# Performance work log

Hardware: AMD Instinct MI355X
Metric: run time of the kernel (lower is better)

Reference implementation:

```python
import jax, jax.numpy as jnp
import numpy as np
from jax.scipy.special import betainc

B, N, F_IN, D = 128, 50, 64, 64
E = N * (N - 1)          # fully-connected directed graph (no self loops)
S = N - 1                # number of ablation submodels
BN_ = B * N
EPS = 1e-5
NEG = jnp.float32(-1e9)
ALPHA = 0.05
SLOPE = 0.2              # LeakyReLU negative slope in GAT attention


def _build_graph():
    # edges grouped by target p: (c, p) for all c != p
    dst = np.repeat(np.arange(N), N - 1)
    src = np.concatenate([np.concatenate([np.arange(p), np.arange(p + 1, N)]) for p in range(N)])
    return src.astype(np.int64), dst.astype(np.int64)


def setup_inputs():
    key = jax.random.key(0)
    k = jax.random.split(key, 16)
    src, dst = _build_graph()
    edge_index = jnp.asarray(np.stack([src, dst]))
    offs = np.repeat(np.arange(B) * N, E)
    # batched edge list (get_batch_edge_index) + self loops appended (GraphLayer add_self_loops)
    src_b = jnp.asarray(np.concatenate([np.tile(src, B) + offs, np.arange(BN_)]))
    dst_b = jnp.asarray(np.concatenate([np.tile(dst, B) + offs, np.arange(BN_)]))
    # submodel s (s>=1) removes, for each target p, its (s-1)-th incoming neighbor (edge order)
    masks = np.ones((S + 1, E), dtype=bool)
    rem = np.empty((S, N), dtype=np.int64)
    for s in range(S):
        for p in range(N):
            e = p * (N - 1) + s
            masks[s + 1, e] = False
            rem[s, p] = e
    g = lambda kk, sh, sc: jax.random.normal(kk, sh, jnp.float32) * sc
    return dict(
        data=g(k[0], (B, N, F_IN), 1.0),
        labels=g(k[1], (B, N), 1.0),
        edge_index=edge_index,
        src_b=src_b, dst_b=dst_b,
        submodel_masks=jnp.asarray(masks),
        removed_edge_id=jnp.asarray(rem),
        emb=g(k[2], (N, D), 0.2),
        W_lin=g(k[3], (F_IN, D), F_IN ** -0.5),
        att_i=g(k[4], (D,), D ** -0.5), att_j=g(k[5], (D,), D ** -0.5),
        att_em_i=g(k[6], (D,), D ** -0.5), att_em_j=g(k[7], (D,), D ** -0.5),
        gat_bias=jnp.zeros((D,), jnp.float32),
        bn1_g=jnp.ones((D,), jnp.float32), bn1_b=jnp.zeros((D,), jnp.float32),
        bn1_rm=jnp.zeros((D,), jnp.float32), bn1_rv=jnp.ones((D,), jnp.float32),
        bn2_g=jnp.ones((D,), jnp.float32), bn2_b=jnp.zeros((D,), jnp.float32),
        bn2_rm=jnp.zeros((D,), jnp.float32), bn2_rv=jnp.ones((D,), jnp.float32),
        out_w=g(k[8], (D, 1), D ** -0.5), out_b=jnp.zeros((1,), jnp.float32),
    )


def reference(data, labels, edge_index, src_b, dst_b, submodel_masks, removed_edge_id,
              emb, W_lin, att_i, att_j, att_em_i, att_em_j, gat_bias,
              bn1_g, bn1_b, bn1_rm, bn1_rv, bn2_g, bn2_b, bn2_rm, bn2_rv, out_w, out_b):
    x_flat = data.reshape(BN_, F_IN)
    emb_nodes = jnp.tile(emb, (B, 1))            # all_embeddings = embedding.repeat(batch,1)

    def gnn(mask_E, train):
        # GDN-style GraphLayer: lin -> per-edge attn on (x||emb) keys -> segment softmax over dst
        emask = jnp.concatenate([jnp.tile(mask_E, B), jnp.ones(BN_, bool)])  # self loops kept
        h = x_flat @ W_lin                                  # [BN_, D]
        s_i = h @ att_i + emb_nodes @ att_em_i              # per-node dst score (key_i . att_i_cat)
        s_j = h @ att_j + emb_nodes @ att_em_j              # per-node src score
        logits = jax.nn.leaky_relu(s_i[dst_b] + s_j[src_b], SLOPE)
        logits = jnp.where(emask, logits, NEG)
        m = jax.ops.segment_max(logits, dst_b, num_segments=BN_)
        p = jnp.where(emask, jnp.exp(logits - m[dst_b]), 0.0)
        denom = jax.ops.segment_sum(p, dst_b, num_segments=BN_)
        alpha = p / denom[dst_b]
        out = jax.ops.segment_sum(alpha[:, None] * h[src_b], dst_b, num_segments=BN_) + gat_bias
        if train:
            mu, var = out.mean(0), out.var(0)               # BatchNorm1d training stats
        else:
            mu, var = bn1_rm, bn1_rv                        # eval mode (causal-edge search)
        return jax.nn.relu((out - mu) / jnp.sqrt(var + EPS) * bn1_g + bn1_b)

    def head(gcn, train):
        x3 = gcn.reshape(B, N, D) * emb[None]               # mul by node embedding
        if train:
            mu, var = x3.mean((0, 1)), x3.var((0, 1))       # BN over (B, N) per channel D
        else:
            mu, var = bn2_rm, bn2_rv
        xn = jax.nn.relu((x3 - mu) / jnp.sqrt(var + EPS) * bn2_g + bn2_b)
        return (xn @ out_w + out_b)[..., 0]                 # OutLayer (layer_num=1) -> [B,N]

    # --- causal ANOVA pruning: S+1 submodel forwards in eval mode (torch.no_grad) ---
    def body(_, mask_E):
        return None, head(gnn(mask_E, False), False)
    _, preds = jax.lax.scan(body, None, submodel_masks)     # [S+1, B, N]
    R = labels[None] - preds
    a, b = R[1:], R[0]                                      # ablated / full-graph residuals
    ma, mb = a.mean(1), b.mean(0)                           # [S,N], [N]
    grand = 0.5 * (ma + mb)
    ssb = B * ((ma - grand) ** 2 + (mb - grand) ** 2)       # between-group SS (df1=1)
    ssw = ((a - ma[:, None, :]) ** 2).sum(1) + ((b - mb) ** 2).sum(0)
    df2 = jnp.float32(2 * B - 2)
    fstat = ssb / (ssw / df2)
    pval = betainc(df2 / 2, 0.5, df2 / (df2 + fstat))       # sf of F(1, 2B-2) == f_oneway p
    prune = (pval > ALPHA).reshape(-1)                      # [S*N] == [E]
    keep = jnp.ones(E, bool).at[removed_edge_id.reshape(-1)].set(~prune)
    keep = jax.lax.stop_gradient(keep)

    # --- final forward on causally-learned graph (training-mode BN, dropout = identity) ---
    return head(gnn(keep, True), True)                      # [B, N]
```

## Files before the change

### kernel.cpp

```cpp
#include <hip/hip_runtime.h>
#include <math.h>

#define B_   128
#define N_   50
#define FIN  64
#define D_   64
#define BN   6400
#define EPSF 1e-5f
#define FCRIT 3.8783305f

__device__ __forceinline__ float wsum(float v){
#pragma unroll
  for(int o=32;o>0;o>>=1) v += __shfl_xor(v,o);
  return v;
}
__device__ __forceinline__ float wmax(float v){
#pragma unroll
  for(int o=32;o>0;o>>=1) v = fmaxf(v,__shfl_xor(v,o));
  return v;
}
__device__ __forceinline__ float leaky(float x){ return x >= 0.f ? x : 0.2f*x; }

__global__ __launch_bounds__(256) void k0_prep(
    const float* __restrict__ bn1_g, const float* __restrict__ bn1_b,
    const float* __restrict__ bn1_rm, const float* __restrict__ bn1_rv,
    const float* __restrict__ bn2_g, const float* __restrict__ bn2_b,
    const float* __restrict__ bn2_rm, const float* __restrict__ bn2_rv,
    const float* __restrict__ gat_bias, const float* __restrict__ out_w,
    float4* __restrict__ hc4, float* __restrict__ hci2g,
    float* __restrict__ stats_raw){
  int t = threadIdx.x;
  stats_raw[t] = 0.f;
  if(t < 64){
    float i1g = bn1_g[t]/sqrtf(bn1_rv[t]+EPSF);
    float i2g = bn2_g[t]/sqrtf(bn2_rv[t]+EPSF);
    float C1 = i1g*gat_bias[t] + bn1_b[t] - bn1_rm[t]*i1g;
    float C2 = bn2_b[t] - bn2_rm[t]*i2g;
    hc4[t] = make_float4(i1g, C1, C2, out_w[t]);
    hci2g[t] = i2g;
  }
}

__global__ __launch_bounds__(256) void k1_lin(
    const float* __restrict__ x, const float* __restrict__ W,
    const float* __restrict__ emb,
    const float* __restrict__ att_i, const float* __restrict__ att_j,
    const float* __restrict__ att_em_i, const float* __restrict__ att_em_j,
    float* __restrict__ h, float* __restrict__ s_i, float* __restrict__ s_j){
  __shared__ float wl[FIN*D_];
  __shared__ float xl[8*FIN];
  int tid = threadIdx.x;
  const float4* W4 = (const float4*)W;
  float4* wl4 = (float4*)wl;
  for(int i=tid;i<FIN*D_/4;i+=256) wl4[i] = W4[i];
  int r0 = blockIdx.x*8;
  { const float4* x4 = (const float4*)(x + (size_t)r0*FIN);
    float4* xl4 = (float4*)xl;
    for(int i=tid;i<8*FIN/4;i+=256) xl4[i] = x4[i]; }
  __syncthreads();
  int w = tid>>6, d = tid&63;
  float acc0 = 0.f, acc1 = 0.f;
#pragma unroll
  for(int k=0;k<FIN;k++){
    float wv = wl[k*D_+d];
    acc0 = fmaf(xl[(w*2+0)*FIN+k], wv, acc0);
    acc1 = fmaf(xl[(w*2+1)*FIN+k], wv, acc1);
  }
  float ai = att_i[d], aj = att_j[d], aei = att_em_i[d], aej = att_em_j[d];
#pragma unroll
  for(int j=0;j<2;j++){
    int r = r0 + w*2 + j;
    float acc = j ? acc1 : acc0;
    h[(size_t)r*D_+d] = acc;
    int n = r % N_;
    float e = emb[n*D_+d];
    float si = wsum(acc*ai + e*aei);
    float sj = wsum(acc*aj + e*aej);
    if(d==0){ s_i[r]=si; s_j[r]=sj; }
  }
}

__global__ __launch_bounds__(256) void k2_preds(
    const float* __restrict__ h, const float* __restrict__ s_i,
    const float* __restrict__ s_j, const float* __restrict__ emb,
    const float* __restrict__ out_b,
    const float4* __restrict__ hc4, const float* __restrict__ hci2g,
    float* __restrict__ preds){
  __shared__ float hT[64*53];
  __shared__ float el[4*64];
  __shared__ float2 wc[4*64];
  int b = blockIdx.y, tid = threadIdx.x;
  const float* hb = h + (size_t)b*N_*D_;
  for(int i=tid;i<N_*D_;i+=256) hT[(i&63)*53 + (i>>6)] = hb[i];
  __syncthreads();
  int w = tid>>6, lane = tid&63;
  int p = blockIdx.x*4 + w;
  if(p >= N_) return;
  float sip = s_i[b*N_+p];
  float L = -3.0e38f;
  if(lane < N_) L = leaky(sip + s_j[b*N_+lane]);
  float M = wmax(L);
  float e = (lane < N_) ? expf(L - M) : 0.f;
  float Dden = wsum(e);
  el[w*64+lane] = e;
  float S = 0.f;
  const float* hTd = &hT[lane*53];
  const float* elw = &el[w*64];
#pragma unroll 10
  for(int q=0;q<N_;q++) S = fmaf(elw[q], hTd[q], S);
  float Em = emb[p*D_+lane]*hci2g[lane];
  wc[w*64+lane] = make_float2(S, Em);
  float er = 0.f; int r = 0;
  if(lane >= 1 && lane < N_){
    int s = lane-1; r = s + (s>=p ? 1 : 0); er = el[w*64+r];
  }
  float den  = Dden - er;
  float beta = 1.f/den;
  float alpha = er*beta;
  float acc = out_b[0];
  const float2* wcw = &wc[w*64];
#pragma unroll 8
  for(int d=0;d<64;d++){
    float4 hc = hc4[d];
    float2 se = wcw[d];
    float hrd = hT[d*53 + r];
    float o  = fmaf(-alpha, hrd, se.x*beta);
    float g  = fmaxf(fmaf(hc.x, o, hc.y), 0.f);
    float xn = fmaxf(fmaf(g, se.y, hc.z), 0.f);
    acc = fmaf(xn, hc.w, acc);
  }
  if(lane < N_) preds[((size_t)p*B_ + b)*64 + lane] = acc;
}

__global__ __launch_bounds__(64) void k3_ftest(
    const float* __restrict__ labels, const float* __restrict__ preds,
    int* __restrict__ keep){
  int blk = blockIdx.x;
  int s = blk / N_, p = blk % N_;
  int t = threadIdx.x;
  float l0 = labels[t*N_+p];
  float l1 = labels[(t+64)*N_+p];
  float a0 = l0 - preds[((size_t)p*B_ + t   )*64 + (s+1)];
  float a1 = l1 - preds[((size_t)p*B_ + t+64)*64 + (s+1)];
  float b0 = l0 - preds[((size_t)p*B_ + t   )*64];
  float b1 = l1 - preds[((size_t)p*B_ + t+64)*64];
  float ma = wsum(a0+a1)*(1.f/B_);
  float mb = wsum(b0+b1)*(1.f/B_);
  float da0=a0-ma, da1=a1-ma, db0=b0-mb, db1=b1-mb;
  float ssw = wsum(da0*da0 + da1*da1 + db0*db0 + db1*db1);
  float g  = 0.5f*(ma+mb);
  float dA = ma-g, dB = mb-g;
  float ssb = (float)B_ * (dA*dA + dB*dB);
  float f = ssb / (ssw / 254.0f);
  int kv = (f < FCRIT) ? 0 : 1;
  if(t==0) keep[p*(N_-1)+s] = kv;
}

__global__ __launch_bounds__(256) void k4a_out(
    const float* __restrict__ h, const float* __restrict__ s_i,
    const float* __restrict__ s_j, const int* __restrict__ keep,
    const float* __restrict__ gat_bias, float* __restrict__ out_raw){
  __shared__ float hT[64*53];
  __shared__ float al[4*64];
  int b = blockIdx.y, tid = threadIdx.x;
  const float* hb = h + (size_t)b*N_*D_;
  for(int i=tid;i<N_*D_;i+=256) hT[(i&63)*53 + (i>>6)] = hb[i];
  __syncthreads();
  int w = tid>>6, lane = tid&63;
  int p = blockIdx.x*4 + w;
  if(p >= N_) return;
  float sip = s_i[b*N_+p];
  float L = -3.0e38f; bool allowed = false;
  if(lane < N_){
    float Lr = leaky(sip + s_j[b*N_+lane]);
    if(lane == p) allowed = true;
    else { int idx = (lane < p) ? lane : lane-1; allowed = keep[p*(N_-1)+idx] != 0; }
    L = allowed ? Lr : -1.0e9f;
  }
  float M = wmax(L);
  float e = allowed ? expf(L - M) : 0.f;
  float D = wsum(e);
  al[w*64+lane] = e;
  float invD = 1.f/D;
  float o = 0.f;
  const float* hTd = &hT[lane*53];
  const float* alw = &al[w*64];
#pragma unroll 10
  for(int q=0;q<N_;q++) o = fmaf(alw[q], hTd[q], o);
  out_raw[((size_t)b*N_+p)*D_ + lane] = o*invD + gat_bias[lane];
}

__global__ __launch_bounds__(256) void k4b1_stats(
    const float* __restrict__ out_raw, float* __restrict__ stats_raw){
  __shared__ float2 red[4][64];
  int tid = threadIdx.x, w = tid>>6, lane = tid&63;
  int r0 = blockIdx.x*64;
  float s1=0.f, s2=0.f;
  for(int i=w;i<64;i+=4){
    float o = out_raw[(size_t)(r0+i)*D_ + lane];
    s1 += o; s2 = fmaf(o,o,s2);
  }
  red[w][lane] = make_float2(s1,s2);
  __syncthreads();
  if(w==0){
    float2 a=red[0][lane], b=red[1][lane], c=red[2][lane], d=red[3][lane];
    atomicAdd(&stats_raw[lane],      a.x+b.x+c.x+d.x);
    atomicAdd(&stats_raw[64+lane],   a.y+b.y+c.y+d.y);
  }
}

__global__ __launch_bounds__(256) void k4b2_stats(
    const float* __restrict__ out_raw, const float* __restrict__ emb,
    const float* __restrict__ bn1_g, const float* __restrict__ bn1_b,
    float* __restrict__ stats_raw){
  __shared__ float2 red[4][64];
  int tid = threadIdx.x, w = tid>>6, lane = tid&63;
  int r0 = blockIdx.x*64;
  float mu1  = stats_raw[lane]     * (1.f/BN);
  float var1 = stats_raw[64+lane]  * (1.f/BN) - mu1*mu1;
  float A = bn1_g[lane]/sqrtf(var1+EPSF);
  float C = bn1_b[lane] - mu1*A;
  float s1=0.f, s2=0.f;
  for(int i=w;i<64;i+=4){
    int r = r0+i;
    float o = out_raw[(size_t)r*D_ + lane];
    float g = fmaxf(fmaf(A,o,C), 0.f);
    float x3 = g*emb[(r%N_)*D_ + lane];
    s1 += x3; s2 = fmaf(x3,x3,s2);
  }
  red[w][lane] = make_float2(s1,s2);
  __syncthreads();
  if(w==0){
    float2 a=red[0][lane], b=red[1][lane], c=red[2][lane], d=red[3][lane];
    atomicAdd(&stats_raw[128+lane],  a.x+b.x+c.x+d.x);
    atomicAdd(&stats_raw[192+lane],  a.y+b.y+c.y+d.y);
  }
}

__global__ __launch_bounds__(256) void k4c_final(
    const float* __restrict__ out_raw, const float* __restrict__ emb,
    const float* __restrict__ bn1_g, const float* __restrict__ bn1_b,
    const float* __restrict__ bn2_g, const float* __restrict__ bn2_b,
    const float* __restrict__ out_w, const float* __restrict__ out_b,
    const float* __restrict__ stats_raw, float* __restrict__ outp){
  int tid = threadIdx.x, w = tid>>6, lane = tid&63;
  float mu1  = stats_raw[lane]     * (1.f/BN);
  float var1 = stats_raw[64+lane]  * (1.f/BN) - mu1*mu1;
  float mu2  = stats_raw[128+lane] * (1.f/BN);
  float var2 = stats_raw[192+lane] * (1.f/BN) - mu2*mu2;
  float A1 = bn1_g[lane]/sqrtf(var1+EPSF);
  float C1 = bn1_b[lane] - mu1*A1;
  float A2 = bn2_g[lane]/sqrtf(var2+EPSF);
  float C2 = bn2_b[lane] - mu2*A2;
  float ow = out_w[lane], ob = out_b[0];
#pragma unroll
  for(int j=0;j<4;j++){
    int r = blockIdx.x*16 + w*4 + j;
    float o = out_raw[(size_t)r*D_ + lane];
    float g = fmaxf(fmaf(A1,o,C1), 0.f);
    float x3 = g*emb[(r%N_)*D_ + lane];
    float xn = fmaxf(fmaf(A2,x3,C2), 0.f);
    float pr = wsum(xn*ow);
    if(lane==0) outp[r] = pr + ob;
  }
}

extern "C" void kernel_launch(void* const* d_in, const int* in_sizes, int n_in,
                              void* d_out, int out_size, void* d_ws, size_t ws_size,
                              hipStream_t stream){
  (void)in_sizes; (void)n_in; (void)out_size; (void)ws_size;
  const float* data     = (const float*)d_in[0];
  const float* labels   = (const float*)d_in[1];
  const float* emb      = (const float*)d_in[7];
  const float* W_lin    = (const float*)d_in[8];
  const float* att_i    = (const float*)d_in[9];
  const float* att_j    = (const float*)d_in[10];
  const float* att_em_i = (const float*)d_in[11];
  const float* att_em_j = (const float*)d_in[12];
  const float* gat_bias = (const float*)d_in[13];
  const float* bn1_g    = (const float*)d_in[14];
  const float* bn1_b    = (const float*)d_in[15];
  const float* bn1_rm   = (const float*)d_in[16];
  const float* bn1_rv   = (const float*)d_in[17];
  const float* bn2_g    = (const float*)d_in[18];
  const float* bn2_b    = (const float*)d_in[19];
  const float* bn2_rm   = (const float*)d_in[20];
  const float* bn2_rv   = (const float*)d_in[21];
  const float* out_w    = (const float*)d_in[22];
  const float* out_b    = (const float*)d_in[23];

  float* ws      = (float*)d_ws;
  float* h       = ws;
  float* s_i     = ws + 409600;
  float* s_j     = ws + 416000;
  float* preds   = ws + 422400;
  float* out_raw = ws + 422400;
  int*   keep    = (int*)(ws + 832000);
  float* stats   = ws + 834560;
  float4* hc4    = (float4*)(ws + 834816);
  float* hci2g   = ws + 835072;
  float* outp    = (float*)d_out;

  hipLaunchKernelGGL(k0_prep, dim3(1), dim3(256), 0, stream,
                     bn1_g, bn1_b, bn1_rm, bn1_rv, bn2_g, bn2_b, bn2_rm, bn2_rv,
                     gat_bias, out_w, hc4, hci2g, stats);
  hipLaunchKernelGGL(k1_lin, dim3(BN/8), dim3(256), 0, stream,
                     data, W_lin, emb, att_i, att_j, att_em_i, att_em_j, h, s_i, s_j);
  hipLaunchKernelGGL(k2_preds, dim3(13, B_), dim3(256), 0, stream,
                     h, s_i, s_j, emb, out_b, hc4, hci2g, preds);
  hipLaunchKernelGGL(k3_ftest, dim3((N_-1)*N_), dim3(64), 0, stream,
                     labels, preds, keep);
  hipLaunchKernelGGL(k4a_out, dim3(13, B_), dim3(256), 0, stream,
                     h, s_i, s_j, keep, gat_bias, out_raw);
  hipLaunchKernelGGL(k4b1_stats, dim3(BN/64), dim3(256), 0, stream,
                     out_raw, stats);
  hipLaunchKernelGGL(k4b2_stats, dim3(BN/64), dim3(256), 0, stream,
                     out_raw, emb, bn1_g, bn1_b, stats);
  hipLaunchKernelGGL(k4c_final, dim3(BN/16), dim3(256), 0, stream,
                     out_raw, emb, bn1_g, bn1_b, bn2_g, bn2_b, out_w, out_b, stats, outp);
}
```

Before: 157.1 us.

## Fuse F-test into output kernel via atomic residual moments; merge prep and stats

The preds kernel now accumulates per-(target, submodel) residual sum and sum of squares with atomics, so the large preds buffer is no longer written. The separate F-test kernel is removed and the keep decision is computed inside the final attention kernel. That kernel also accumulates the first BatchNorm statistics into 8 slotted partial buffers. The prep work and buffer zeroing move into block 0 of the linear kernel, and the attention kernels go to 512-thread blocks covering 8 targets each. This drops three launches and a round trip through global memory. In exchange it adds atomic contention and computes variance from raw moments, which is less numerically stable.

```diff
diff --git a/kernel.cpp b/kernel.cpp
--- a/kernel.cpp
+++ b/kernel.cpp
@@ -21,32 +21,19 @@
 }
 __device__ __forceinline__ float leaky(float x){ return x >= 0.f ? x : 0.2f*x; }
 
-__global__ __launch_bounds__(256) void k0_prep(
+__global__ __launch_bounds__(256) void k1_lin(
+    const float* __restrict__ x, const float* __restrict__ W,
+    const float* __restrict__ emb,
+    const float* __restrict__ att_i, const float* __restrict__ att_j,
+    const float* __restrict__ att_em_i, const float* __restrict__ att_em_j,
     const float* __restrict__ bn1_g, const float* __restrict__ bn1_b,
     const float* __restrict__ bn1_rm, const float* __restrict__ bn1_rv,
     const float* __restrict__ bn2_g, const float* __restrict__ bn2_b,
     const float* __restrict__ bn2_rm, const float* __restrict__ bn2_rv,
     const float* __restrict__ gat_bias, const float* __restrict__ out_w,
-    float4* __restrict__ hc4, float* __restrict__ hci2g,
-    float* __restrict__ stats_raw){
-  int t = threadIdx.x;
-  stats_raw[t] = 0.f;
-  if(t < 64){
-    float i1g = bn1_g[t]/sqrtf(bn1_rv[t]+EPSF);
-    float i2g = bn2_g[t]/sqrtf(bn2_rv[t]+EPSF);
-    float C1 = i1g*gat_bias[t] + bn1_b[t] - bn1_rm[t]*i1g;
-    float C2 = bn2_b[t] - bn2_rm[t]*i2g;
-    hc4[t] = make_float4(i1g, C1, C2, out_w[t]);
-    hci2g[t] = i2g;
-  }
-}
-
-__global__ __launch_bounds__(256) void k1_lin(
-    const float* __restrict__ x, const float* __restrict__ W,
-    const float* __restrict__ emb,
-    const float* __restrict__ att_i, const float* __restrict__ att_j,
-    const float* __restrict__ att_em_i, const float* __restrict__ att_em_j,
-    float* __restrict__ h, float* __restrict__ s_i, float* __restrict__ s_j){
+    float* __restrict__ h, float* __restrict__ s_i, float* __restrict__ s_j,
+    float2* __restrict__ acc, float* __restrict__ statz ,
+    float4* __restrict__ hc4, float* __restrict__ hci2g){
   __shared__ float wl[FIN*D_];
   __shared__ float xl[8*FIN];
   int tid = threadIdx.x;
@@ -70,31 +57,43 @@
 #pragma unroll
   for(int j=0;j<2;j++){
     int r = r0 + w*2 + j;
-    float acc = j ? acc1 : acc0;
-    h[(size_t)r*D_+d] = acc;
+    float a_ = j ? acc1 : acc0;
+    h[(size_t)r*D_+d] = a_;
     int n = r % N_;
     float e = emb[n*D_+d];
-    float si = wsum(acc*ai + e*aei);
-    float sj = wsum(acc*aj + e*aej);
+    float si = wsum(a_*ai + e*aei);
+    float sj = wsum(a_*aj + e*aej);
     if(d==0){ s_i[r]=si; s_j[r]=sj; }
   }
-}
-
-__global__ __launch_bounds__(256) void k2_preds(
+  if(blockIdx.x==0){
+    for(int i=tid;i<N_*N_;i+=256) acc[i] = make_float2(0.f,0.f);
+    for(int i=tid;i<2048;i+=256)  statz[i] = 0.f;
+    if(tid < 64){
+      float i1g = bn1_g[tid]/sqrtf(bn1_rv[tid]+EPSF);
+      float i2g = bn2_g[tid]/sqrtf(bn2_rv[tid]+EPSF);
+      float C1 = i1g*gat_bias[tid] + bn1_b[tid] - bn1_rm[tid]*i1g;
+      float C2 = bn2_b[tid] - bn2_rm[tid]*i2g;
+      hc4[tid] = make_float4(i1g, C1, C2, out_w[tid]);
+      hci2g[tid] = i2g;
+    }
+  }
+}
+
+__global__ __launch_bounds__(512) void k2_preds(
     const float* __restrict__ h, const float* __restrict__ s_i,
-    const float* __restrict__ s_j, const float* __restrict__ emb,
-    const float* __restrict__ out_b,
+    const float* __restrict__ s_j, const float* __restrict__ labels,
+    const float* __restrict__ emb, const float* __restrict__ out_b,
     const float4* __restrict__ hc4, const float* __restrict__ hci2g,
-    float* __restrict__ preds){
+    float2* __restrict__ acc){
   __shared__ float hT[64*53];
-  __shared__ float el[4*64];
-  __shared__ float2 wc[4*64];
+  __shared__ float el[8*64];
+  __shared__ float2 wc[8*64];
   int b = blockIdx.y, tid = threadIdx.x;
   const float* hb = h + (size_t)b*N_*D_;
-  for(int i=tid;i<N_*D_;i+=256) hT[(i&63)*53 + (i>>6)] = hb[i];
+  for(int i=tid;i<N_*D_;i+=512) hT[(i&63)*53 + (i>>6)] = hb[i];
   __syncthreads();
   int w = tid>>6, lane = tid&63;
-  int p = blockIdx.x*4 + w;
+  int p = blockIdx.x*8 + w;
   if(p >= N_) return;
   float sip = s_i[b*N_+p];
   float L = -3.0e38f;
@@ -108,16 +107,14 @@
   const float* elw = &el[w*64];
 #pragma unroll 10
   for(int q=0;q<N_;q++) S = fmaf(elw[q], hTd[q], S);
-  float Em = emb[p*D_+lane]*hci2g[lane];
-  wc[w*64+lane] = make_float2(S, Em);
+  wc[w*64+lane] = make_float2(S, emb[p*D_+lane]*hci2g[lane]);
   float er = 0.f; int r = 0;
   if(lane >= 1 && lane < N_){
     int s = lane-1; r = s + (s>=p ? 1 : 0); er = el[w*64+r];
   }
-  float den  = Dden - er;
-  float beta = 1.f/den;
+  float beta = 1.f/(Dden - er);
   float alpha = er*beta;
-  float acc = out_b[0];
+  float acc_ = out_b[0];
   const float2* wcw = &wc[w*64];
 #pragma unroll 8
   for(int d=0;d<64;d++){
@@ -127,99 +124,91 @@
     float o  = fmaf(-alpha, hrd, se.x*beta);
     float g  = fmaxf(fmaf(hc.x, o, hc.y), 0.f);
     float xn = fmaxf(fmaf(g, se.y, hc.z), 0.f);
-    acc = fmaf(xn, hc.w, acc);
-  }
-  if(lane < N_) preds[((size_t)p*B_ + b)*64 + lane] = acc;
-}
-
-__global__ __launch_bounds__(64) void k3_ftest(
-    const float* __restrict__ labels, const float* __restrict__ preds,
-    int* __restrict__ keep){
-  int blk = blockIdx.x;
-  int s = blk / N_, p = blk % N_;
-  int t = threadIdx.x;
-  float l0 = labels[t*N_+p];
-  float l1 = labels[(t+64)*N_+p];
-  float a0 = l0 - preds[((size_t)p*B_ + t   )*64 + (s+1)];
-  float a1 = l1 - preds[((size_t)p*B_ + t+64)*64 + (s+1)];
-  float b0 = l0 - preds[((size_t)p*B_ + t   )*64];
-  float b1 = l1 - preds[((size_t)p*B_ + t+64)*64];
-  float ma = wsum(a0+a1)*(1.f/B_);
-  float mb = wsum(b0+b1)*(1.f/B_);
-  float da0=a0-ma, da1=a1-ma, db0=b0-mb, db1=b1-mb;
-  float ssw = wsum(da0*da0 + da1*da1 + db0*db0 + db1*db1);
-  float g  = 0.5f*(ma+mb);
-  float dA = ma-g, dB = mb-g;
-  float ssb = (float)B_ * (dA*dA + dB*dB);
-  float f = ssb / (ssw / 254.0f);
-  int kv = (f < FCRIT) ? 0 : 1;
-  if(t==0) keep[p*(N_-1)+s] = kv;
-}
-
-__global__ __launch_bounds__(256) void k4a_out(
+    acc_ = fmaf(xn, hc.w, acc_);
+  }
+  if(lane < N_){
+    float resid = labels[b*N_+p] - acc_;
+    atomicAdd(&acc[p*N_+lane].x, resid);
+    atomicAdd(&acc[p*N_+lane].y, resid*resid);
+  }
+}
+
+__global__ __launch_bounds__(512) void k4a_out(
     const float* __restrict__ h, const float* __restrict__ s_i,
-    const float* __restrict__ s_j, const int* __restrict__ keep,
-    const float* __restrict__ gat_bias, float* __restrict__ out_raw){
+    const float* __restrict__ s_j, const float2* __restrict__ acc,
+    const float* __restrict__ gat_bias,
+    float* __restrict__ out_raw, float* __restrict__ stats1){
   __shared__ float hT[64*53];
-  __shared__ float al[4*64];
+  __shared__ float al[8*64];
+  __shared__ int   keepL[8*64];
+  __shared__ float2 red[8][64];
   int b = blockIdx.y, tid = threadIdx.x;
   const float* hb = h + (size_t)b*N_*D_;
-  for(int i=tid;i<N_*D_;i+=256) hT[(i&63)*53 + (i>>6)] = hb[i];
+  for(int i=tid;i<N_*D_;i+=512) hT[(i&63)*53 + (i>>6)] = hb[i];
   __syncthreads();
   int w = tid>>6, lane = tid&63;
-  int p = blockIdx.x*4 + w;
-  if(p >= N_) return;
-  float sip = s_i[b*N_+p];
-  float L = -3.0e38f; bool allowed = false;
-  if(lane < N_){
-    float Lr = leaky(sip + s_j[b*N_+lane]);
-    if(lane == p) allowed = true;
-    else { int idx = (lane < p) ? lane : lane-1; allowed = keep[p*(N_-1)+idx] != 0; }
-    L = allowed ? Lr : -1.0e9f;
-  }
-  float M = wmax(L);
-  float e = allowed ? expf(L - M) : 0.f;
-  float D = wsum(e);
-  al[w*64+lane] = e;
-  float invD = 1.f/D;
+  int p = blockIdx.x*8 + w;
+  bool act = (p < N_);
   float o = 0.f;
-  const float* hTd = &hT[lane*53];
-  const float* alw = &al[w*64];
+  if(act){
+    int kb = 1;
+    if(lane < N_-1){
+      float2 A2 = acc[p*N_ + lane + 1];
+      float2 B2 = acc[p*N_];
+      float ma = A2.x*(1.f/B_), mb = B2.x*(1.f/B_);
+      float ssw = (A2.y - (float)B_*ma*ma) + (B2.y - (float)B_*mb*mb);
+      float dmb = ma - mb;
+      float f = (64.f*dmb*dmb) / (ssw*(1.f/254.f));
+      kb = (f < FCRIT) ? 0 : 1;
+    }
+    keepL[w*64+lane] = kb;
+    float sip = s_i[b*N_+p];
+    float L = -3.0e38f; bool allowed = false;
+    if(lane < N_){
+      float Lr = leaky(sip + s_j[b*N_+lane]);
+      if(lane == p) allowed = true;
+      else { int idx = (lane < p) ? lane : lane-1; allowed = keepL[w*64+idx] != 0; }
+      L = allowed ? Lr : -1.0e9f;
+    }
+    float M = wmax(L);
+    float e = allowed ? expf(L - M) : 0.f;
+    float Dn = wsum(e);
+    al[w*64+lane] = e;
+    float invD = 1.f/Dn;
+    float s = 0.f;
+    const float* hTd = &hT[lane*53];
+    const float* alw = &al[w*64];
 #pragma unroll 10
-  for(int q=0;q<N_;q++) o = fmaf(alw[q], hTd[q], o);
-  out_raw[((size_t)b*N_+p)*D_ + lane] = o*invD + gat_bias[lane];
-}
-
-__global__ __launch_bounds__(256) void k4b1_stats(
-    const float* __restrict__ out_raw, float* __restrict__ stats_raw){
+    for(int q=0;q<N_;q++) s = fmaf(alw[q], hTd[q], s);
+    o = s*invD + gat_bias[lane];
+    out_raw[((size_t)b*N_+p)*D_ + lane] = o;
+  }
+  red[w][lane] = act ? make_float2(o, o*o) : make_float2(0.f, 0.f);
+  __syncthreads();
+  if(w==0){
+    float s1=0.f, s2=0.f;
+#pragma unroll
+    for(int k=0;k<8;k++){ float2 v = red[k][lane]; s1+=v.x; s2+=v.y; }
+    int slot = b & 7;
+    atomicAdd(&stats1[slot*128 + lane],      s1);
+    atomicAdd(&stats1[slot*128 + 64 + lane], s2);
+  }
+}
+
+__global__ __launch_bounds__(256) void k4b_stats(
+    const float* __restrict__ out_raw, const float* __restrict__ emb,
+    const float* __restrict__ bn1_g, const float* __restrict__ bn1_b,
+    const float* __restrict__ stats1, float* __restrict__ stats2){
   __shared__ float2 red[4][64];
   int tid = threadIdx.x, w = tid>>6, lane = tid&63;
-  int r0 = blockIdx.x*64;
-  float s1=0.f, s2=0.f;
-  for(int i=w;i<64;i+=4){
-    float o = out_raw[(size_t)(r0+i)*D_ + lane];
-    s1 += o; s2 = fmaf(o,o,s2);
-  }
-  red[w][lane] = make_float2(s1,s2);
-  __syncthreads();
-  if(w==0){
-    float2 a=red[0][lane], b=red[1][lane], c=red[2][lane], d=red[3][lane];
-    atomicAdd(&stats_raw[lane],      a.x+b.x+c.x+d.x);
-    atomicAdd(&stats_raw[64+lane],   a.y+b.y+c.y+d.y);
-  }
-}
-
-__global__ __launch_bounds__(256) void k4b2_stats(
-    const float* __restrict__ out_raw, const float* __restrict__ emb,
-    const float* __restrict__ bn1_g, const float* __restrict__ bn1_b,
-    float* __restrict__ stats_raw){
-  __shared__ float2 red[4][64];
-  int tid = threadIdx.x, w = tid>>6, lane = tid&63;
-  int r0 = blockIdx.x*64;
-  float mu1  = stats_raw[lane]     * (1.f/BN);
-  float var1 = stats_raw[64+lane]  * (1.f/BN) - mu1*mu1;
+  float t1=0.f, t2=0.f;
+#pragma unroll
+  for(int k=0;k<8;k++){ t1 += stats1[k*128+lane]; t2 += stats1[k*128+64+lane]; }
+  float mu1  = t1*(1.f/BN);
+  float var1 = t2*(1.f/BN) - mu1*mu1;
   float A = bn1_g[lane]/sqrtf(var1+EPSF);
   float C = bn1_b[lane] - mu1*A;
+  int r0 = blockIdx.x*64;
   float s1=0.f, s2=0.f;
   for(int i=w;i<64;i+=4){
     int r = r0+i;
@@ -232,8 +221,9 @@
   __syncthreads();
   if(w==0){
     float2 a=red[0][lane], b=red[1][lane], c=red[2][lane], d=red[3][lane];
-    atomicAdd(&stats_raw[128+lane],  a.x+b.x+c.x+d.x);
-    atomicAdd(&stats_raw[192+lane],  a.y+b.y+c.y+d.y);
+    int slot = blockIdx.x & 7;
+    atomicAdd(&stats2[slot*128 + lane],      a.x+b.x+c.x+d.x);
+    atomicAdd(&stats2[slot*128 + 64 + lane], a.y+b.y+c.y+d.y);
   }
 }
 
@@ -242,12 +232,17 @@
     const float* __restrict__ bn1_g, const float* __restrict__ bn1_b,
     const float* __restrict__ bn2_g, const float* __restrict__ bn2_b,
     const float* __restrict__ out_w, const float* __restrict__ out_b,
-    const float* __restrict__ stats_raw, float* __restrict__ outp){
+    const float* __restrict__ stats1, const float* __restrict__ stats2,
+    float* __restrict__ outp){
   int tid = threadIdx.x, w = tid>>6, lane = tid&63;
-  float mu1  = stats_raw[lane]     * (1.f/BN);
-  float var1 = stats_raw[64+lane]  * (1.f/BN) - mu1*mu1;
-  float mu2  = stats_raw[128+lane] * (1.f/BN);
-  float var2 = stats_raw[192+lane] * (1.f/BN) - mu2*mu2;
+  float t1=0.f, t2=0.f, t3=0.f, t4=0.f;
+#pragma unroll
+  for(int k=0;k<8;k++){
+    t1 += stats1[k*128+lane]; t2 += stats1[k*128+64+lane];
+    t3 += stats2[k*128+lane]; t4 += stats2[k*128+64+lane];
+  }
+  float mu1  = t1*(1.f/BN), var1 = t2*(1.f/BN) - mu1*mu1;
+  float mu2  = t3*(1.f/BN), var2 = t4*(1.f/BN) - mu2*mu2;
   float A1 = bn1_g[lane]/sqrtf(var1+EPSF);
   float C1 = bn1_b[lane] - mu1*A1;
   float A2 = bn2_g[lane]/sqrtf(var2+EPSF);
@@ -289,33 +284,29 @@
   const float* out_w    = (const float*)d_in[22];
   const float* out_b    = (const float*)d_in[23];
 
-  float* ws      = (float*)d_ws;
-  float* h       = ws;
-  float* s_i     = ws + 409600;
-  float* s_j     = ws + 416000;
-  float* preds   = ws + 422400;
-  float* out_raw = ws + 422400;
-  int*   keep    = (int*)(ws + 832000);
-  float* stats   = ws + 834560;
-  float4* hc4    = (float4*)(ws + 834816);
-  float* hci2g   = ws + 835072;
-  float* outp    = (float*)d_out;
-
-  hipLaunchKernelGGL(k0_prep, dim3(1), dim3(256), 0, stream,
+  float*  ws      = (float*)d_ws;
+  float*  h       = ws;
+  float*  s_i     = ws + 409600;
+  float*  s_j     = ws + 416000;
+  float*  out_raw = ws + 422400;
+  float2* acc     = (float2*)(ws + 832000);
+  float*  stats1  = ws + 837000;
+  float*  stats2  = ws + 838024;
+  float4* hc4     = (float4*)(ws + 839048);
+  float*  hci2g   = ws + 839304;
+  float*  outp    = (float*)d_out;
+
+  hipLaunchKernelGGL(k1_lin, dim3(BN/8), dim3(256), 0, stream,
+                     data, W_lin, emb, att_i, att_j, att_em_i, att_em_j,
                      bn1_g, bn1_b, bn1_rm, bn1_rv, bn2_g, bn2_b, bn2_rm, bn2_rv,
-                     gat_bias, out_w, hc4, hci2g, stats);
-  hipLaunchKernelGGL(k1_lin, dim3(BN/8), dim3(256), 0, stream,
-                     data, W_lin, emb, att_i, att_j, att_em_i, att_em_j, h, s_i, s_j);
-  hipLaunchKernelGGL(k2_preds, dim3(13, B_), dim3(256), 0, stream,
-                     h, s_i, s_j, emb, out_b, hc4, hci2g, preds);
-  hipLaunchKernelGGL(k3_ftest, dim3((N_-1)*N_), dim3(64), 0, stream,
-                     labels, preds, keep);
-  hipLaunchKernelGGL(k4a_out, dim3(13, B_), dim3(256), 0, stream,
-                     h, s_i, s_j, keep, gat_bias, out_raw);
-  hipLaunchKernelGGL(k4b1_stats, dim3(BN/64), dim3(256), 0, stream,
-                     out_raw, stats);
-  hipLaunchKernelGGL(k4b2_stats, dim3(BN/64), dim3(256), 0, stream,
-                     out_raw, emb, bn1_g, bn1_b, stats);
+                     gat_bias, out_w, h, s_i, s_j, acc, stats1, hc4, hci2g);
+  hipLaunchKernelGGL(k2_preds, dim3(7, B_), dim3(512), 0, stream,
+                     h, s_i, s_j, labels, emb, out_b, hc4, hci2g, acc);
+  hipLaunchKernelGGL(k4a_out, dim3(7, B_), dim3(512), 0, stream,
+                     h, s_i, s_j, acc, gat_bias, out_raw, stats1);
+  hipLaunchKernelGGL(k4b_stats, dim3(BN/64), dim3(256), 0, stream,
+                     out_raw, emb, bn1_g, bn1_b, stats1, stats2);
   hipLaunchKernelGGL(k4c_final, dim3(BN/16), dim3(256), 0, stream,
-                     out_raw, emb, bn1_g, bn1_b, bn2_g, bn2_b, out_w, out_b, stats, outp);
-}
+                     out_raw, emb, bn1_g, bn1_b, bn2_g, bn2_b, out_w, out_b,
+                     stats1, stats2, outp);
+}
```

Measured after the change: 142.9 us. 9.0% less time.
